# Kernel tuning notes

Hardware: AMD Instinct MI355X
Metric: run time of the kernel (lower is better)

Reference implementation:

```python
import jax, jax.numpy as jnp
import numpy as np

DIM = 384
HEADS = 8


def setup_inputs() -> dict:
    key = jax.random.key(0)
    ks = jax.random.split(key, 8)
    d = DIM
    return {
        "x": jax.random.normal(ks[0], (4, d, 128, 128), jnp.float32),
        "message": jax.random.normal(ks[1], (4, d, 128, 128), jnp.float32),
        "temperature": jnp.ones((HEADS, 1, 1), jnp.float32),
        "qkv_w": jax.random.normal(ks[2], (3 * d, d), jnp.float32) * 0.02,   # 1x1 conv weight
        "dw_w": jax.random.normal(ks[3], (3 * d, 1, 3, 3), jnp.float32) * 0.02,  # depthwise 3x3
        "proj_w": jax.random.normal(ks[4], (d, d), jnp.float32) * 0.02,     # project_out 1x1
        "lin_w": jax.random.normal(ks[5], (d, 2 * d), jnp.float32) * 0.02,  # nn.Linear weight [out,in]
        "lin_b": jnp.zeros((d,), jnp.float32),
    }


def _qkv_branch(t, qkv_w, dw_w):
    # 1x1 conv (pointwise) then depthwise 3x3, groups = 3*dim
    y = jnp.einsum('oc,bchw->bohw', qkv_w, t)
    y = jax.lax.conv_general_dilated(
        y, dw_w, window_strides=(1, 1), padding='SAME',
        dimension_numbers=('NCHW', 'OIHW', 'NCHW'),
        feature_group_count=dw_w.shape[0])
    return jnp.split(y, 3, axis=1)  # q, k, v each [b, dim, h, w]


def _to_heads(t):
    b, c, h, w = t.shape
    return t.reshape(b, HEADS, c // HEADS, h * w)  # [b, head, c, n]


def _l2norm(t):
    # torch F.normalize(dim=-1, eps=1e-12)
    n = jnp.sqrt(jnp.sum(t * t, axis=-1, keepdims=True))
    return t / jnp.maximum(n, 1e-12)


def reference(x, message, temperature, qkv_w, dw_w, proj_w, lin_w, lin_b):
    b, c, h, w = x.shape
    q, k, v = (_to_heads(t) for t in _qkv_branch(x, qkv_w, dw_w))
    q_m, k_m, v_m = (_to_heads(t) for t in _qkv_branch(message, qkv_w, dw_w))

    k_c = jnp.concatenate([k, k_m], axis=2)   # [b, head, 2c, n]
    v_c = jnp.concatenate([v, v_m], axis=2)

    q = _l2norm(q)
    k_c = _l2norm(k_c)
    q_m = _l2norm(q_m)

    # channel attention: [b, head, c, 2c]
    attn1 = jax.nn.softmax(jnp.einsum('bhcn,bhdn->bhcd', q, k_c) * temperature, axis=-1)
    attn2 = jax.nn.softmax(jnp.einsum('bhcn,bhdn->bhcd', q_m, k_c) * temperature, axis=-1)

    out1 = jnp.einsum('bhcd,bhdn->bhcn', attn1, v_c)  # [b, head, c, n]
    out2 = jnp.einsum('bhcd,bhdn->bhcn', attn2, v_c)

    # 'b head c (h w) -> b (h w) (head c)'
    out1 = out1.transpose(0, 3, 1, 2).reshape(b, h * w, c)
    out2 = out2.transpose(0, 3, 1, 2).reshape(b, h * w, c)

    cat = jnp.concatenate([out1, out2], axis=2)  # [b, n, 2c]
    out = cat @ lin_w.T + lin_b                  # [b, n, c]

    # 'b (h w) c -> b c h w'
    out = out.transpose(0, 2, 1).reshape(b, c, h, w)
    out = jnp.einsum('oc,bchw->bohw', proj_w, out)
    return out
```

## Files before the change

### kernel.cpp

```cpp
#include <hip/hip_runtime.h>

typedef unsigned short u16;
typedef unsigned int u32;

#define BATCH 4
#define CDIM 384
#define IMG 128
#define HW 16384
#define QKVC 1152
#define NHEADS 8
#define CHD 48
#define DD2 96
#define KFIN 768

typedef __attribute__((ext_vector_type(8))) short bf16x8;
typedef __attribute__((ext_vector_type(4))) float f32x4;

__device__ __forceinline__ u16 f2bf(float f){
  union { float f; u32 u; } v; v.f = f;
  u32 u = v.u;
  u32 r = (u + 0x7fffu + ((u >> 16) & 1u)) >> 16;
  return (u16)r;
}
__device__ __forceinline__ float bf2f(u16 h){
  union { u32 u; float f; } v; v.u = ((u32)h) << 16;
  return v.f;
}

#define OFF_QKVX  ((size_t)0)
#define OFF_QKVM  ((size_t)150994944)
#define OFF_T     ((size_t)301989888)
#define OFF_SSQ   ((size_t)339738624)
#define OFF_S     ((size_t)339775488)
#define OFF_ATTN  ((size_t)340955136)
#define OFF_AFINB ((size_t)342134784)
#define OFF_W2    ((size_t)344494080)
#define OFF_B2    ((size_t)345673728)
#define OFF_WB    ((size_t)345675264)

typedef __attribute__((address_space(1))) const u32 gas_u32;
typedef __attribute__((address_space(3))) u32 las_u32;
__device__ __forceinline__ void gl_lds16(const u16* g, u16* l){
  __builtin_amdgcn_global_load_lds((gas_u32*)g, (las_u32*)l, 16, 0, 0);
}

__device__ __forceinline__ u16* t_row(u16* T0, u16* qkvm, int par, int ch){
  if (par == 0) return T0 + (size_t)ch * HW;
  int bq = ch / 384;
  int rr = ch - bq * 384;
  return qkvm + ((size_t)bq * QKVC + 2 * CDIM + rr) * HW;
}

__global__ void __launch_bounds__(256) k_w2(const float* __restrict__ proj,
                                            const float* __restrict__ lin,
                                            const float* __restrict__ linb,
                                            const float* __restrict__ qkvw,
                                            float* __restrict__ W2,
                                            float* __restrict__ b2,
                                            u16* __restrict__ Wb){
  int idx = blockIdx.x * 256 + threadIdx.x;
  if (idx < CDIM * KFIN){
    int o = idx / KFIN, d = idx % KFIN;
    float acc = 0.f;
    for (int c = 0; c < CDIM; c++)
      acc = fmaf(proj[o * CDIM + c], lin[c * KFIN + d], acc);
    W2[idx] = acc;
  }
  if (idx < CDIM){
    float acc = 0.f;
    for (int c = 0; c < CDIM; c++)
      acc = fmaf(proj[idx * CDIM + c], linb[c], acc);
    b2[idx] = acc;
  }
  if (idx < QKVC * CDIM) Wb[idx] = f2bf(qkvw[idx]);
}

__device__ __forceinline__ void loadrow(const u16* __restrict__ src, int r, int cg, float* o){
  if ((unsigned)r >= IMG){
    #pragma unroll
    for (int i = 0; i < 18; i++) o[i] = 0.f;
    return;
  }
  const u16* p = src + (size_t)r * IMG + cg * 16;
  uint4 v0 = *(const uint4*)p;
  uint4 v1 = *(const uint4*)(p + 8);
  u32 ww[8] = {v0.x, v0.y, v0.z, v0.w, v1.x, v1.y, v1.z, v1.w};
  #pragma unroll
  for (int i = 0; i < 8; i++){
    union { u32 u; float f; } lo, hi;
    lo.u = ww[i] << 16;
    hi.u = ww[i] & 0xffff0000u;
    o[1 + 2 * i] = lo.f;
    o[2 + 2 * i] = hi.f;
  }
  o[0]  = (cg > 0) ? bf2f(p[-1]) : 0.f;
  o[17] = (cg < 7) ? bf2f(p[16]) : 0.f;
}

__global__ void __launch_bounds__(256) k_stage(
    int t, int nlog, int npw, int ndw,
    const u16* __restrict__ Wb, u16* __restrict__ Bt,
    u16* __restrict__ T0, u16* __restrict__ qkvx, u16* __restrict__ qkvm,
    const float* __restrict__ x, const float* __restrict__ msg,
    const float* __restrict__ dww, float* __restrict__ ssq,
    float* __restrict__ S){
  __shared__ __align__(16) u16 smem[16384];
  int bid = blockIdx.x;
  int tid = threadIdx.x;

  if (bid < nlog){
    int idx = bid;
    int b = idx >> 8;
    int nc = idx & 31;
    int h = (idx >> 5) & 7;
    int w = tid >> 6, lane = tid & 63;
    int wy = w >> 1, wx = w & 1;
    int lm = lane & 15, quad = lane >> 4;

    const u16* ap[3]; const u16* bp[3];
    #pragma unroll
    for (int i = 0; i < 3; i++){
      int g = wy * 48 + i * 16 + lm;
      int c = (g < 48) ? g : g - 48;
      ap[i] = ((g < 48) ? qkvx : qkvm) + ((size_t)b * QKVC + h * CHD + c) * HW;
      int d = wx * 48 + i * 16 + lm;
      int cc = (d < 48) ? d : d - 48;
      bp[i] = ((d < 48) ? qkvx : qkvm) + ((size_t)b * QKVC + CDIM + h * CHD + cc) * HW;
    }
    f32x4 acc[3][3];
    #pragma unroll
    for (int i = 0; i < 3; i++)
      #pragma unroll
      for (int j = 0; j < 3; j++) acc[i][j] = (f32x4){0.f,0.f,0.f,0.f};

    int nbeg = nc * 512 + quad * 8;
    int nend = nc * 512 + 512;
    for (int n = nbeg; n < nend; n += 64){
      bf16x8 af0[3], bf0[3], af1[3], bf1[3];
      #pragma unroll
      for (int i = 0; i < 3; i++){
        af0[i] = *(const bf16x8*)(ap[i] + n);
        af1[i] = *(const bf16x8*)(ap[i] + n + 32);
      }
      #pragma unroll
      for (int j = 0; j < 3; j++){
        bf0[j] = *(const bf16x8*)(bp[j] + n);
        bf1[j] = *(const bf16x8*)(bp[j] + n + 32);
      }
      #pragma unroll
      for (int i = 0; i < 3; i++)
        #pragma unroll
        for (int j = 0; j < 3; j++)
          acc[i][j] = __builtin_amdgcn_mfma_f32_16x16x32_bf16(af0[i], bf0[j], acc[i][j], 0, 0, 0);
      #pragma unroll
      for (int i = 0; i < 3; i++)
        #pragma unroll
        for (int j = 0; j < 3; j++)
          acc[i][j] = __builtin_amdgcn_mfma_f32_16x16x32_bf16(af1[i], bf1[j], acc[i][j], 0, 0, 0);
    }
    #pragma unroll
    for (int i = 0; i < 3; i++){
      #pragma unroll
      for (int r = 0; r < 4; r++){
        int g = wy * 48 + i * 16 + quad * 4 + r;
        int iq = (g >= 48) ? 1 : 0;
        int c = iq ? g - 48 : g;
        float* Sp = S + (((size_t)(iq * BATCH + b) * NHEADS + h) * CHD + c) * DD2;
        #pragma unroll
        for (int j = 0; j < 3; j++)
          atomicAdd(&Sp[wx * 48 + j * 16 + lm], acc[i][j][r]);
      }
    }

  } else if (bid < nlog + npw){
    int pb = bid - nlog;
    int z = t - 1, par = z & 1;
    const u16* B = Bt + (size_t)z * HW * CDIM;
    u16* As = smem;
    u16* Bs = smem + 8192;
    int swz = (pb & 7) * 144 + (pb >> 3);
    int bx = swz % 9, by = swz / 9;
    int m0 = bx * 128, n0 = by * 128;
    int w = tid >> 6, lane = tid & 63;
    int wy = w >> 1, wx = w & 1;
    int lm = lane & 15, q = lane >> 4;

    int srow = w * 16 + (lane >> 2);
    int scol = (lane & 3) * 8;
    const u16* ga = Wb + (size_t)(m0 + srow) * CDIM + scol;
    const u16* gb = B + (size_t)(n0 + srow) * CDIM + scol;
    u16* la = As + srow * 32 + scol;
    u16* lb = Bs + srow * 32 + scol;

    f32x4 acc[4][4];
    #pragma unroll
    for (int i = 0; i < 4; i++)
      #pragma unroll
      for (int j = 0; j < 4; j++) acc[i][j] = (f32x4){0.f,0.f,0.f,0.f};

#define PW_STAGE(buf, k0) do{ \
      gl_lds16(ga + (k0),             la + (buf) * 4096); \
      gl_lds16(ga + 64*CDIM + (k0),   la + (buf) * 4096 + 2048); \
      gl_lds16(gb + (k0),             lb + (buf) * 4096); \
      gl_lds16(gb + 64*CDIM + (k0),   lb + (buf) * 4096 + 2048); \
    }while(0)

    PW_STAGE(0, 0);
    __syncthreads();
    int cur = 0;
    for (int kt = 0; kt < 12; kt++){
      if (kt < 11) PW_STAGE(cur ^ 1, (kt + 1) * 32);
      bf16x8 af[4], bfr[4];
      #pragma unroll
      for (int i = 0; i < 4; i++)
        af[i] = *(const bf16x8*)&As[cur * 4096 + (wy * 64 + i * 16 + lm) * 32 + q * 8];
      #pragma unroll
      for (int j = 0; j < 4; j++)
        bfr[j] = *(const bf16x8*)&Bs[cur * 4096 + (wx * 64 + j * 16 + lm) * 32 + q * 8];
      #pragma unroll
      for (int i = 0; i < 4; i++)
        #pragma unroll
        for (int j = 0; j < 4; j++)
          acc[i][j] = __builtin_amdgcn_mfma_f32_16x16x32_bf16(af[i], bfr[j], acc[i][j], 0, 0, 0);
      __syncthreads();
      cur ^= 1;
    }
#undef PW_STAGE
    #pragma unroll
    for (int i = 0; i < 4; i++){
      #pragma unroll
      for (int r = 0; r < 4; r++){
        int row = m0 + wy * 64 + i * 16 + q * 4 + r;
        u16* cp = t_row(T0, qkvm, par, row) + n0 + wx * 64 + lm;
        #pragma unroll
        for (int j = 0; j < 4; j++)
          cp[j * 16] = f2bf(acc[i][j][r]);
      }
    }

  } else if (bid < nlog + npw + ndw){
    int ch = bid - nlog - npw;
    int z = t - 2, par = z & 1;
    const u16* src = t_row(T0, qkvm, par, ch);
    u16* dst;
    if (ch < 2 * CDIM){
      u16* qd = ((z >> 2) ? qkvm : qkvx) + (size_t)(z & 3) * QKVC * HW;
      dst = qd + (size_t)ch * HW;
    } else {
      dst = Bt + (size_t)z * HW * CDIM + (size_t)(ch - 2 * CDIM) * HW;
    }
    float w[9];
    #pragma unroll
    for (int t9 = 0; t9 < 9; t9++) w[t9] = dww[ch * 9 + t9];
    int rg = tid >> 3, cg = tid & 7;
    int r0 = rg * 4;
    float ra[18], rb[18], rc[18];
    loadrow(src, r0 - 1, cg, ra);
    loadrow(src, r0,     cg, rb);
    float ss = 0.f;
    #pragma unroll
    for (int rr = 0; rr < 4; rr++){
      int r = r0 + rr;
      loadrow(src, r + 1, cg, rc);
      u32 pk[8];
      #pragma unroll
      for (int xx = 0; xx < 16; xx++){
        float a2 = w[0] * ra[xx];
        a2 = fmaf(w[1], ra[xx + 1], a2);
        a2 = fmaf(w[2], ra[xx + 2], a2);
        a2 = fmaf(w[3], rb[xx],     a2);
        a2 = fmaf(w[4], rb[xx + 1], a2);
        a2 = fmaf(w[5], rb[xx + 2], a2);
        a2 = fmaf(w[6], rc[xx],     a2);
        a2 = fmaf(w[7], rc[xx + 1], a2);
        a2 = fmaf(w[8], rc[xx + 2], a2);
        ss = fmaf(a2, a2, ss);
        u16 hv = f2bf(a2);
        if (xx & 1) pk[xx >> 1] |= (u32)hv << 16;
        else        pk[xx >> 1]  = (u32)hv;
      }
      *(uint4*)(dst + (size_t)r * IMG + cg * 16)     = *(uint4*)&pk[0];
      *(uint4*)(dst + (size_t)r * IMG + cg * 16 + 8) = *(uint4*)&pk[4];
      #pragma unroll
      for (int ii = 0; ii < 18; ii++){ ra[ii] = rb[ii]; rb[ii] = rc[ii]; }
    }
    if (ch < 2 * CDIM){
      float* red = (float*)smem;
      red[tid] = ss;
      __syncthreads();
      for (int s = 128; s > 0; s >>= 1){
        if (tid < s) red[tid] += red[tid + s];
        __syncthreads();
      }
      if (tid == 0) ssq[(size_t)z * QKVC + ch] = red[0];
    }

  } else {
    int cb = bid - nlog - npw - ndw;
    int z = t;
    const float* src = (z < 4 ? x : msg) + (size_t)(z & 3) * CDIM * HW;
    u16* dstz = Bt + (size_t)z * HW * CDIM;
    int n0 = (cb & 127) * 128;
    int c0 = (cb >> 7) * 64;
    u16 (*tile)[130] = (u16(*)[130])smem;
    #pragma unroll
    for (int i = 0; i < 8; i++){
      int c = (tid >> 5) + i * 8;
      int nq = tid & 31;
      float4 v = *(const float4*)(src + (size_t)(c0 + c) * HW + n0 + nq * 4);
      u32 p0 = (u32)f2bf(v.x) | ((u32)f2bf(v.y) << 16);
      u32 p1 = (u32)f2bf(v.z) | ((u32)f2bf(v.w) << 16);
      *(u32*)&tile[c][nq * 4]     = p0;
      *(u32*)&tile[c][nq * 4 + 2] = p1;
    }
    __syncthreads();
    #pragma unroll
    for (int u = 0; u < 2; u++){
      int idx = tid + u * 256;
      int n = idx >> 2, j = idx & 3;
      u32 pk[8];
      #pragma unroll
      for (int p = 0; p < 8; p++)
        pk[p] = (u32)tile[j * 16 + 2 * p][n] | ((u32)tile[j * 16 + 2 * p + 1][n] << 16);
      u16* dp = dstz + (size_t)(n0 + n) * CDIM + c0 + j * 16;
      *(uint4*)dp       = *(uint4*)&pk[0];
      *(uint4*)(dp + 8) = *(uint4*)&pk[4];
    }
  }
}

__global__ void __launch_bounds__(256) k_tail(u16* __restrict__ qkvx,
                                              u16* __restrict__ qkvm,
                                              float* __restrict__ S,
                                              const u16* __restrict__ Bt){
  __shared__ u16 tile[48][136];
  int bid = blockIdx.x;
  int tid = threadIdx.x;

  if (bid < 256){
    int b = 3;
    int nc = bid & 31;
    int h = bid >> 5;
    int w = tid >> 6, lane = tid & 63;
    int wy = w >> 1, wx = w & 1;
    int lm = lane & 15, quad = lane >> 4;

    const u16* ap[3]; const u16* bp[3];
    #pragma unroll
    for (int i = 0; i < 3; i++){
      int g = wy * 48 + i * 16 + lm;
      int c = (g < 48) ? g : g - 48;
      ap[i] = ((g < 48) ? qkvx : qkvm) + ((size_t)b * QKVC + h * CHD + c) * HW;
      int d = wx * 48 + i * 16 + lm;
      int cc = (d < 48) ? d : d - 48;
      bp[i] = ((d < 48) ? qkvx : qkvm) + ((size_t)b * QKVC + CDIM + h * CHD + cc) * HW;
    }
    f32x4 acc[3][3];
    #pragma unroll
    for (int i = 0; i < 3; i++)
      #pragma unroll
      for (int j = 0; j < 3; j++) acc[i][j] = (f32x4){0.f,0.f,0.f,0.f};

    int nbeg = nc * 512 + quad * 8;
    int nend = nc * 512 + 512;
    for (int n = nbeg; n < nend; n += 64){
      bf16x8 af0[3], bf0[3], af1[3], bf1[3];
      #pragma unroll
      for (int i = 0; i < 3; i++){
        af0[i] = *(const bf16x8*)(ap[i] + n);
        af1[i] = *(const bf16x8*)(ap[i] + n + 32);
      }
      #pragma unroll
      for (int j = 0; j < 3; j++){
        bf0[j] = *(const bf16x8*)(bp[j] + n);
        bf1[j] = *(const bf16x8*)(bp[j] + n + 32);
      }
      #pragma unroll
      for (int i = 0; i < 3; i++)
        #pragma unroll
        for (int j = 0; j < 3; j++)
          acc[i][j] = __builtin_amdgcn_mfma_f32_16x16x32_bf16(af0[i], bf0[j], acc[i][j], 0, 0, 0);
      #pragma unroll
      for (int i = 0; i < 3; i++)
        #pragma unroll
        for (int j = 0; j < 3; j++)
          acc[i][j] = __builtin_amdgcn_mfma_f32_16x16x32_bf16(af1[i], bf1[j], acc[i][j], 0, 0, 0);
    }
    #pragma unroll
    for (int i = 0; i < 3; i++){
      #pragma unroll
      for (int r = 0; r < 4; r++){
        int g = wy * 48 + i * 16 + quad * 4 + r;
        int iq = (g >= 48) ? 1 : 0;
        int c = iq ? g - 48 : g;
        float* Sp = S + (((size_t)(iq * BATCH + b) * NHEADS + h) * CHD + c) * DD2;
        #pragma unroll
        for (int j = 0; j < 3; j++)
          atomicAdd(&Sp[wx * 48 + j * 16 + lm], acc[i][j][r]);
      }
    }
  } else {
    int v = bid - 256;
    int nb = v & 127;
    int h = (v >> 7) & 7;
    int z = v >> 10;
    int inp = z >> 2, b = z & 3;
    const u16* vcn = Bt + (size_t)z * HW * CDIM;
    int n0 = nb * 128;
    u16* vt = (h < 4 ? qkvx : qkvm) + ((size_t)b * QKVC + 2 * CDIM) * HW;
    int dbase = (h & 3) * 96 + inp * 48;
    #pragma unroll
    for (int j = 0; j < 3; j++){
      int i = tid + j * 256;
      int row = i >> 4, c8 = i & 15;
      uint4 vv = *(const uint4*)(vcn + (size_t)(h * 48 + row) * HW + n0 + c8 * 8);
      *(uint4*)&tile[row][c8 * 8] = vv;
    }
    __syncthreads();
    int n = tid >> 1, half = tid & 1;
    u16* dstp = vt + (size_t)(n0 + n) * CDIM + dbase + half * 24;
    #pragma unroll
    for (int u = 0; u < 3; u++){
      u32 pk[4];
      #pragma unroll
      for (int p = 0; p < 4; p++){
        int c = half * 24 + u * 8 + p * 2;
        pk[p] = (u32)tile[c][n] | ((u32)tile[c + 1][n] << 16);
      }
      *(uint4*)(dstp + u * 8) = *(uint4*)pk;
    }
  }
}

__global__ void __launch_bounds__(128) k_softmax(const float* __restrict__ S,
                                                 const float* __restrict__ ssq,
                                                 const float* __restrict__ temp,
                                                 float* __restrict__ attn){
  int row = blockIdx.x;
  int c = row % CHD;
  int h = (row / CHD) % NHEADS;
  int b = (row / (CHD * NHEADS)) % BATCH;
  int iq = row / (CHD * NHEADS * BATCH);
  int tid = threadIdx.x;
  __shared__ float sh[128];
  const float* Sp = S + (size_t)row * DD2;
  float ssq_q = ssq[(iq * BATCH + b) * QKVC + h * CHD + c];
  float nq = fmaxf(sqrtf(ssq_q), 1e-12f);
  float tmp = temp[h];
  float logit = -1e30f;
  int d = tid;
  if (d < DD2){
    float ssq_k = ssq[((d < CHD ? 0 : 1) * BATCH + b) * QKVC + CDIM + h * CHD + (d % CHD)];
    float nk = fmaxf(sqrtf(ssq_k), 1e-12f);
    logit = Sp[d] * tmp / (nq * nk);
  }
  sh[tid] = logit; __syncthreads();
  for (int s = 64; s > 0; s >>= 1){
    if (tid < s) sh[tid] = fmaxf(sh[tid], sh[tid + s]);
    __syncthreads();
  }
  float mx = sh[0]; __syncthreads();
  float e = (d < DD2) ? expf(logit - mx) : 0.f;
  sh[tid] = e; __syncthreads();
  for (int s = 64; s > 0; s >>= 1){
    if (tid < s) sh[tid] += sh[tid + s];
    __syncthreads();
  }
  float sum = sh[0];
  if (d < DD2) attn[(size_t)row * DD2 + d] = e / sum;
}

__global__ void __launch_bounds__(128) k_mmat(const float* __restrict__ attn,
                                              const float* __restrict__ W2,
                                              u16* __restrict__ AfinB){
  int oz = blockIdx.x;
  int h = blockIdx.y;
  int b = blockIdx.z;
  __shared__ float a1[CHD * DD2];
  __shared__ float a2[CHD * DD2];
  int tid = threadIdx.x;
  const float* A1 = attn + ((size_t)(0 * BATCH + b) * NHEADS + h) * CHD * DD2;
  const float* A2 = attn + ((size_t)(1 * BATCH + b) * NHEADS + h) * CHD * DD2;
  for (int i = tid; i < CHD * DD2; i += 128){ a1[i] = A1[i]; a2[i] = A2[i]; }
  __syncthreads();
  int e = tid;
  if (e < DD2){
    for (int oo = 0; oo < 8; oo++){
      int o = oz * 8 + oo;
      float acc = 0.f;
      #pragma unroll 4
      for (int cc = 0; cc < CHD; cc++){
        acc = fmaf(W2[o * KFIN + h * CHD + cc],        a1[cc * DD2 + e], acc);
        acc = fmaf(W2[o * KFIN + CDIM + h * CHD + cc], a2[cc * DD2 + e], acc);
      }
      AfinB[((size_t)b * CDIM + o) * KFIN + h * DD2 + e] = f2bf(acc);
    }
  }
}

__global__ void __launch_bounds__(256) k_fin(const u16* __restrict__ AfB,
                                             const u16* __restrict__ qkvx,
                                             const u16* __restrict__ qkvm,
                                             const float* __restrict__ b2,
                                             float* __restrict__ out){
  __shared__ __align__(16) u16 As[2 * 4096];
  __shared__ __align__(16) u16 Bs[2 * 4096];
  int orig = blockIdx.x;
  int swz = (orig & 7) * 192 + (orig >> 3);
  int m = swz % 3;
  int rest = swz / 3;
  int n0 = (rest & 127) * 128;
  int bz = rest >> 7;
  int m0 = m * 128;
  int tid = threadIdx.x;
  int w = tid >> 6, lane = tid & 63;
  int wy = w >> 1, wx = w & 1;
  int lm = lane & 15, q = lane >> 4;

  int srow = w * 16 + (lane >> 2);
  int scol = (lane & 3) * 8;
  const u16* A = AfB + (size_t)bz * CDIM * KFIN;
  const u16* ga  = A + (size_t)(m0 + srow) * KFIN + scol;
  const u16* gb0 = qkvx + ((size_t)bz * QKVC + 2 * CDIM) * HW + (size_t)(n0 + srow) * CDIM + scol;
  const u16* gb1 = qkvm + ((size_t)bz * QKVC + 2 * CDIM) * HW + (size_t)(n0 + srow) * CDIM + scol;
  u16* la = As + srow * 32 + scol;
  u16* lb = Bs + srow * 32 + scol;

  f32x4 acc[4][4];
  #pragma unroll
  for (int i = 0; i < 4; i++)
    #pragma unroll
    for (int j = 0; j < 4; j++) acc[i][j] = (f32x4){0.f,0.f,0.f,0.f};

#define FIN_STAGE(buf, t) do{ \
    int hp_ = (t) >= 12; \
    int k0_ = ((t) - hp_ * 12) * 32; \
    const u16* gb_ = hp_ ? gb1 : gb0; \
    gl_lds16(ga + hp_ * CDIM + k0_,            la + (buf) * 4096); \
    gl_lds16(ga + hp_ * CDIM + k0_ + 64*KFIN,  la + (buf) * 4096 + 2048); \
    gl_lds16(gb_ + k0_,                        lb + (buf) * 4096); \
    gl_lds16(gb_ + k0_ + 64*CDIM,              lb + (buf) * 4096 + 2048); \
  }while(0)

  FIN_STAGE(0, 0);
  __syncthreads();
  int cur = 0;
  for (int t = 0; t < 24; t++){
    if (t < 23) FIN_STAGE(cur ^ 1, t + 1);
    bf16x8 af[4], bfr[4];
    #pragma unroll
    for (int i = 0; i < 4; i++)
      af[i] = *(const bf16x8*)&As[cur * 4096 + (wy * 64 + i * 16 + lm) * 32 + q * 8];
    #pragma unroll
    for (int j = 0; j < 4; j++)
      bfr[j] = *(const bf16x8*)&Bs[cur * 4096 + (wx * 64 + j * 16 + lm) * 32 + q * 8];
    #pragma unroll
    for (int i = 0; i < 4; i++)
      #pragma unroll
      for (int j = 0; j < 4; j++)
        acc[i][j] = __builtin_amdgcn_mfma_f32_16x16x32_bf16(af[i], bfr[j], acc[i][j], 0, 0, 0);
    __syncthreads();
    cur ^= 1;
  }
#undef FIN_STAGE
  #pragma unroll
  for (int i = 0; i < 4; i++){
    #pragma unroll
    for (int r = 0; r < 4; r++){
      int row = m0 + wy * 64 + i * 16 + q * 4 + r;
      float bv = b2[row];
      float* cp = out + (size_t)bz * CDIM * HW + (size_t)row * HW + n0 + wx * 64 + lm;
      #pragma unroll
      for (int j = 0; j < 4; j++)
        cp[j * 16] = acc[i][j][r] + bv;
    }
  }
}

extern "C" void kernel_launch(void* const* d_in, const int* in_sizes, int n_in,
                              void* d_out, int out_size, void* d_ws, size_t ws_size,
                              hipStream_t stream){
  const float* x      = (const float*)d_in[0];
  const float* msg    = (const float*)d_in[1];
  const float* temp   = (const float*)d_in[2];
  const float* qkv_w  = (const float*)d_in[3];
  const float* dw_w   = (const float*)d_in[4];
  const float* proj_w = (const float*)d_in[5];
  const float* lin_w  = (const float*)d_in[6];
  const float* lin_b  = (const float*)d_in[7];
  float* out = (float*)d_out;

  char* ws = (char*)d_ws;
  u16*   qkvx  = (u16*)(ws + OFF_QKVX);
  u16*   qkvm  = (u16*)(ws + OFF_QKVM);
  u16*   T0    = (u16*)(ws + OFF_T);
  float* ssq   = (float*)(ws + OFF_SSQ);
  float* S     = (float*)(ws + OFF_S);
  float* attn  = (float*)(ws + OFF_ATTN);
  u16*   AfinB = (u16*)(ws + OFF_AFINB);
  float* W2    = (float*)(ws + OFF_W2);
  float* b2    = (float*)(ws + OFF_B2);
  u16*   Wb    = (u16*)(ws + OFF_WB);

  u16* Bt = (u16*)d_out;

  hipMemsetAsync(ws + OFF_S, 0, (OFF_ATTN - OFF_S), stream);

  k_w2<<<dim3((QKVC * CDIM + 255) / 256), dim3(256), 0, stream>>>(
      proj_w, lin_w, lin_b, qkv_w, W2, b2, Wb);

  for (int t = 0; t < 10; t++){
    int nlog = (t == 9) ? 768 : 0;
    int npw  = (t >= 1 && t <= 8) ? 1152 : 0;
    int ndw  = (t >= 2) ? 1152 : 0;
    int ncvt = (t < 8) ? 768 : 0;
    k_stage<<<dim3(nlog + npw + ndw + ncvt), dim3(256), 0, stream>>>(
        t, nlog, npw, ndw, Wb, Bt, T0, qkvx, qkvm, x, msg, dw_w, ssq, S);
  }

  k_tail<<<dim3(256 + 8192), dim3(256), 0, stream>>>(qkvx, qkvm, S, Bt);
  k_softmax<<<dim3(2 * BATCH * NHEADS * CHD), dim3(128), 0, stream>>>(S, ssq, temp, attn);
  k_mmat<<<dim3(CDIM / 8, NHEADS, BATCH), dim3(128), 0, stream>>>(attn, W2, AfinB);
  k_fin<<<dim3(3 * (HW / 128) * BATCH), dim3(256), 0, stream>>>(
      AfinB, qkvx, qkvm, b2, out);
}
```

Baseline: 821.2 us.

## Fold weight prep into first stage, spread logit blocks across stages, unroll tail

The standalone weight-prep kernel (W2 = proj·lin, the bias fold, and the bf16 conversion of qkv_w) becomes an extra block range in the first pipeline stage. It now runs alongside the input conversion instead of as its own serialized launch. The q·k logit blocks for batches 0–2 move from a single 768-block burst in the last stage to 256 blocks in each of stages 7, 8 and 9, which balances per-stage load. The tail's logit loop now unrolls four 32-wide chunks per iteration for more loads in flight. This relies on each batch's qkv being complete by the stage that reads it, and the deeper unroll raises register pressure.

New measurement: 842.7 us. 2.6% more time.

```diff
diff --git a/kernel.cpp b/kernel.cpp
--- a/kernel.cpp
+++ b/kernel.cpp
@@ -49,30 +49,6 @@
   int bq = ch / 384;
   int rr = ch - bq * 384;
   return qkvm + ((size_t)bq * QKVC + 2 * CDIM + rr) * HW;
-}
-
-__global__ void __launch_bounds__(256) k_w2(const float* __restrict__ proj,
-                                            const float* __restrict__ lin,
-                                            const float* __restrict__ linb,
-                                            const float* __restrict__ qkvw,
-                                            float* __restrict__ W2,
-                                            float* __restrict__ b2,
-                                            u16* __restrict__ Wb){
-  int idx = blockIdx.x * 256 + threadIdx.x;
-  if (idx < CDIM * KFIN){
-    int o = idx / KFIN, d = idx % KFIN;
-    float acc = 0.f;
-    for (int c = 0; c < CDIM; c++)
-      acc = fmaf(proj[o * CDIM + c], lin[c * KFIN + d], acc);
-    W2[idx] = acc;
-  }
-  if (idx < CDIM){
-    float acc = 0.f;
-    for (int c = 0; c < CDIM; c++)
-      acc = fmaf(proj[idx * CDIM + c], linb[c], acc);
-    b2[idx] = acc;
-  }
-  if (idx < QKVC * CDIM) Wb[idx] = f2bf(qkvw[idx]);
 }
 
 __device__ __forceinline__ void loadrow(const u16* __restrict__ src, int r, int cg, float* o){
@@ -98,21 +74,23 @@
 }
 
 __global__ void __launch_bounds__(256) k_stage(
-    int t, int nlog, int npw, int ndw,
+    int t, int nlog, int npw, int ndw, int ncvt,
     const u16* __restrict__ Wb, u16* __restrict__ Bt,
     u16* __restrict__ T0, u16* __restrict__ qkvx, u16* __restrict__ qkvm,
     const float* __restrict__ x, const float* __restrict__ msg,
     const float* __restrict__ dww, float* __restrict__ ssq,
-    float* __restrict__ S){
+    float* __restrict__ S,
+    const float* __restrict__ proj, const float* __restrict__ lin,
+    const float* __restrict__ linb, const float* __restrict__ qkvw,
+    float* __restrict__ W2, float* __restrict__ b2, u16* __restrict__ Wbw){
   __shared__ __align__(16) u16 smem[16384];
   int bid = blockIdx.x;
   int tid = threadIdx.x;
 
   if (bid < nlog){
-    int idx = bid;
-    int b = idx >> 8;
-    int nc = idx & 31;
-    int h = (idx >> 5) & 7;
+    int b = t - 7;
+    int nc = bid & 31;
+    int h = bid >> 5;
     int w = tid >> 6, lane = tid & 63;
     int wy = w >> 1, wx = w & 1;
     int lm = lane & 15, quad = lane >> 4;
@@ -295,7 +273,7 @@
       if (tid == 0) ssq[(size_t)z * QKVC + ch] = red[0];
     }
 
-  } else {
+  } else if (bid < nlog + npw + ndw + ncvt){
     int cb = bid - nlog - npw - ndw;
     int z = t;
     const float* src = (z < 4 ? x : msg) + (size_t)(z & 3) * CDIM * HW;
@@ -326,6 +304,23 @@
       *(uint4*)dp       = *(uint4*)&pk[0];
       *(uint4*)(dp + 8) = *(uint4*)&pk[4];
     }
+
+  } else {
+    int idx = (bid - nlog - npw - ndw - ncvt) * 256 + tid;
+    if (idx < CDIM * KFIN){
+      int o = idx / KFIN, d = idx % KFIN;
+      float acc = 0.f;
+      for (int c = 0; c < CDIM; c++)
+        acc = fmaf(proj[o * CDIM + c], lin[c * KFIN + d], acc);
+      W2[idx] = acc;
+    }
+    if (idx < CDIM){
+      float acc = 0.f;
+      for (int c = 0; c < CDIM; c++)
+        acc = fmaf(proj[idx * CDIM + c], linb[c], acc);
+      b2[idx] = acc;
+    }
+    if (idx < QKVC * CDIM) Wbw[idx] = f2bf(qkvw[idx]);
   }
 }
 
@@ -363,28 +358,23 @@
 
     int nbeg = nc * 512 + quad * 8;
     int nend = nc * 512 + 512;
-    for (int n = nbeg; n < nend; n += 64){
-      bf16x8 af0[3], bf0[3], af1[3], bf1[3];
-      #pragma unroll
-      for (int i = 0; i < 3; i++){
-        af0[i] = *(const bf16x8*)(ap[i] + n);
-        af1[i] = *(const bf16x8*)(ap[i] + n + 32);
-      }
-      #pragma unroll
-      for (int j = 0; j < 3; j++){
-        bf0[j] = *(const bf16x8*)(bp[j] + n);
-        bf1[j] = *(const bf16x8*)(bp[j] + n + 32);
-      }
-      #pragma unroll
-      for (int i = 0; i < 3; i++)
-        #pragma unroll
-        for (int j = 0; j < 3; j++)
-          acc[i][j] = __builtin_amdgcn_mfma_f32_16x16x32_bf16(af0[i], bf0[j], acc[i][j], 0, 0, 0);
-      #pragma unroll
-      for (int i = 0; i < 3; i++)
-        #pragma unroll
-        for (int j = 0; j < 3; j++)
-          acc[i][j] = __builtin_amdgcn_mfma_f32_16x16x32_bf16(af1[i], bf1[j], acc[i][j], 0, 0, 0);
+    for (int n = nbeg; n < nend; n += 128){
+      bf16x8 af[4][3], bfr[4][3];
+      #pragma unroll
+      for (int u = 0; u < 4; u++){
+        #pragma unroll
+        for (int i = 0; i < 3; i++){
+          af[u][i]  = *(const bf16x8*)(ap[i] + n + u * 32);
+          bfr[u][i] = *(const bf16x8*)(bp[i] + n + u * 32);
+        }
+      }
+      #pragma unroll
+      for (int u = 0; u < 4; u++)
+        #pragma unroll
+        for (int i = 0; i < 3; i++)
+          #pragma unroll
+          for (int j = 0; j < 3; j++)
+            acc[i][j] = __builtin_amdgcn_mfma_f32_16x16x32_bf16(af[u][i], bfr[u][j], acc[i][j], 0, 0, 0);
     }
     #pragma unroll
     for (int i = 0; i < 3; i++){
@@ -606,16 +596,15 @@
 
   hipMemsetAsync(ws + OFF_S, 0, (OFF_ATTN - OFF_S), stream);
 
-  k_w2<<<dim3((QKVC * CDIM + 255) / 256), dim3(256), 0, stream>>>(
-      proj_w, lin_w, lin_b, qkv_w, W2, b2, Wb);
-
   for (int t = 0; t < 10; t++){
-    int nlog = (t == 9) ? 768 : 0;
+    int nlog = (t >= 7) ? 256 : 0;
     int npw  = (t >= 1 && t <= 8) ? 1152 : 0;
     int ndw  = (t >= 2) ? 1152 : 0;
     int ncvt = (t < 8) ? 768 : 0;
-    k_stage<<<dim3(nlog + npw + ndw + ncvt), dim3(256), 0, stream>>>(
-        t, nlog, npw, ndw, Wb, Bt, T0, qkvx, qkvm, x, msg, dw_w, ssq, S);
+    int nw2  = (t == 0) ? 1728 : 0;
+    k_stage<<<dim3(nlog + npw + ndw + ncvt + nw2), dim3(256), 0, stream>>>(
+        t, nlog, npw, ndw, ncvt, Wb, Bt, T0, qkvx, qkvm, x, msg, dw_w, ssq, S,
+        proj_w, lin_w, lin_b, qkv_w, W2, b2, Wb);
   }
 
   k_tail<<<dim3(256 + 8192), dim3(256), 0, stream>>>(qkvx, qkvm, S, Bt);
```
